# Kernel optimization log

Hardware: AMD Instinct MI355X
Metric: run time of the kernel (lower is better)

## Reference

```python
import jax, jax.numpy as jnp
import numpy as np

H, W = 40, 40
PC_MIN_X, PC_MIN_Y = -51.2, -51.2
DIM_X, DIM_Y = 102.4, 102.4  # pc_range[3:] - pc_range[:3] (x, y)
EFF_MIN, EFF_MAX = 1.0, 6.0


def _grids():
    # np.meshgrid(range(W), range(H)) with 'xy' indexing, then reshape(-1)
    ww = jnp.tile(jnp.arange(W, dtype=jnp.float32), H)
    hh = jnp.repeat(jnp.arange(H, dtype=jnp.float32), W)
    x = (ww + 0.5) / W * DIM_X + PC_MIN_X
    y = (hh + 0.5) / H * DIM_Y + PC_MIN_Y
    return jnp.stack([x, y], axis=1)  # [G=1600, 2]


def _corners(centers, dims, angles):
    # center_to_corner_box2d: unit-square corners scaled, rotated, translated. [M,4,2]
    cn = jnp.array([[-0.5, -0.5], [-0.5, 0.5], [0.5, 0.5], [0.5, -0.5]], dtype=centers.dtype)
    corners = dims[:, None, :] * cn[None]  # [M,4,2]
    c, s = jnp.cos(angles), jnp.sin(angles)
    rot = jnp.stack([jnp.stack([c, -s], -1), jnp.stack([s, c], -1)], -2)  # [M,2,2]
    corners = jnp.einsum('mij,mkj->mki', rot, corners)
    return corners + centers[:, None, :]


def _points_in_poly(points, corners):
    # points [G,2], corners [4,2] -> [G] bool (inside convex quad, sign-consistent cross)
    edges = jnp.roll(corners, -1, axis=0) - corners  # [4,2]
    rel = points[:, None, :] - corners[None]  # [G,4,2]
    cross = edges[None, :, 0] * rel[..., 1] - edges[None, :, 1] * rel[..., 0]  # [G,4]
    return jnp.all(cross >= 0, axis=1) | jnp.all(cross <= 0, axis=1)


def _assign(grids, corners, centers):
    # Sequential per-box grid assignment with the original's overwrite-to-(-1) dedup rule.
    M = corners.shape[0]

    def step(flag, xs):
        i, crn, ctr = xs
        inside = _points_in_poly(grids, crn)
        dist = jnp.sum((grids - ctr) ** 2, axis=1)
        mask = inside.at[jnp.argmin(dist)].set(True)  # always include nearest grid to center
        all_free = jnp.all((~mask) | (flag == -1))
        new_flag = jnp.where(mask, jnp.where(all_free | (flag == -1), i, -1), flag)
        return new_flag, None

    flag0 = -jnp.ones(grids.shape[0], dtype=jnp.int32)
    flag, _ = jax.lax.scan(step, flag0, (jnp.arange(M, dtype=jnp.int32), corners, centers))
    return flag  # [G]


def _forward(atten_map, gt_bboxes):
    B, G, D = atten_map.shape
    M = gt_bboxes.shape[1]
    grids = _grids()
    centers = gt_bboxes[..., :2]
    l, w = gt_bboxes[..., 3], gt_bboxes[..., 4]
    ratio_l = jnp.clip(DIM_X / W / l, EFF_MIN, EFF_MAX)
    ratio_w = jnp.clip(DIM_Y / H / w, EFF_MIN, EFF_MAX)
    eff_dims = jnp.stack([l * ratio_l, w * ratio_w], axis=-1)  # [B,M,2]
    angles = gt_bboxes[..., 6]
    corners = jax.vmap(_corners)(centers, eff_dims, angles)  # [B,M,4,2]
    flags = jax.vmap(lambda c, ct: _assign(grids, c, ct))(corners, centers)  # [B,G]

    # var over feature dim (torch.var default unbiased, ddof=1) per grid cell
    v = jnp.var(atten_map, axis=2, ddof=1)  # [B,G]
    onehot = (flags[:, :, None] == jnp.arange(M, dtype=flags.dtype)[None, None, :])  # [B,G,M]
    counts = onehot.sum(axis=1)  # [B,M]
    sums = jnp.einsum('bg,bgm->bm', v, onehot.astype(v.dtype))
    means = jnp.where(counts > 0, sums / jnp.maximum(counts, 1).astype(v.dtype), 0.0)
    var_loss = -jnp.sum(means)
    pos_num = jnp.maximum(jnp.sum(counts > 0), 1).astype(v.dtype)
    return var_loss / pos_num


def setup_inputs() -> dict:
    key = jax.random.key(0)
    k1, k2 = jax.random.split(key)
    B, G, D, M = 16, 1600, 2048, 64
    atten_map = jax.random.uniform(k1, (B, G, D), dtype=jnp.float32)
    u = jax.random.uniform(k2, (B, M, 7), dtype=jnp.float32)
    xy = u[..., :2] * 80.0 - 40.0          # centers inside pc_range
    z = u[..., 2:3] * 4.0 - 3.0
    lwh = u[..., 3:6] * 7.0 + 1.0          # box sizes in [1, 8] m
    yaw = u[..., 6:7] * (2.0 * np.pi) - np.pi
    gt_bboxes = jnp.concatenate([xy, z, lwh, yaw], axis=-1)
    return {"atten_map": atten_map, "gt_bboxes": gt_bboxes}


def reference(atten_map, gt_bboxes):
    return _forward(atten_map, gt_bboxes)
```

## Files before the change

### kernel.cpp

```cpp
#include <hip/hip_runtime.h>

#define NB 16
#define NG 1600
#define NM 64
#define ND 2048

typedef float floatx4 __attribute__((ext_vector_type(4)));

__global__ __launch_bounds__(256) void var_kernel(const float* __restrict__ atten,
                                                  float* __restrict__ v,
                                                  float* __restrict__ acc) {
    if (blockIdx.x == 0 && threadIdx.x == 0) {
        acc[0] = 0.0f; acc[1] = 0.0f; ((int*)acc)[2] = 0;
    }
    const int wave = threadIdx.x >> 6;
    const int lane = threadIdx.x & 63;
    const int bg = blockIdx.x * 4 + wave;
    const floatx4* p = (const floatx4*)(atten + (size_t)bg * ND);
    double s = 0.0, ss = 0.0;
#pragma unroll
    for (int k = 0; k < 8; ++k) {
        floatx4 f = __builtin_nontemporal_load(p + lane + 64 * k);
        double x0 = f.x, x1 = f.y, x2 = f.z, x3 = f.w;
        s += (x0 + x1) + (x2 + x3);
        ss += (x0 * x0 + x1 * x1) + (x2 * x2 + x3 * x3);
    }
#pragma unroll
    for (int off = 32; off > 0; off >>= 1) {
        s += __shfl_down(s, off, 64);
        ss += __shfl_down(ss, off, 64);
    }
    if (lane == 0)
        v[bg] = (float)((ss - s * s / (double)ND) / (double)(ND - 1));
}

__device__ __forceinline__ int axis_argmin(float c) {
    float u = (c + 51.2f) / 2.56f - 0.5f;
    int i0 = (int)floorf(u) - 1;
    if (i0 < 0) i0 = 0;
    if (i0 > 37) i0 = 37;
    int best_i = i0;
    float best_d = 3.4e38f;
#pragma unroll
    for (int k = 0; k < 3; ++k) {
        int i = i0 + k;
        float p = (i + 0.5f) / 40.0f * 102.4f - 51.2f;
        float d = p - c;
        float d2 = d * d;
        if (d2 < best_d) { best_d = d2; best_i = i; }
    }
    return best_i;
}

__global__ __launch_bounds__(512) void assign_kernel(const float* __restrict__ gt,
                                                     const float* __restrict__ v,
                                                     float* __restrict__ acc,
                                                     float* __restrict__ out) {
    __shared__ float s_kx[NM][4], s_ky[NM][4];
    __shared__ int   s_gmin[NM];
    __shared__ float s_sum[NM];
    __shared__ int   s_cnt[NM];

    const int b = blockIdx.x;
    const int t = threadIdx.x;
    const float* bb = gt + (size_t)b * NM * 7;

    if (t < NM) {
        const float cx = bb[t * 7 + 0], cy = bb[t * 7 + 1];
        const float l = bb[t * 7 + 3], w = bb[t * 7 + 4];
        const float ang = bb[t * 7 + 6];
        float rl = 2.56f / l; rl = fminf(fmaxf(rl, 1.0f), 6.0f);
        float rw = 2.56f / w; rw = fminf(fmaxf(rw, 1.0f), 6.0f);
        const float el = l * rl, ew = w * rw;
        const float c = cosf(ang), s = sinf(ang);
        const float cnx[4] = {-0.5f, -0.5f, 0.5f, 0.5f};
        const float cny[4] = {-0.5f, 0.5f, 0.5f, -0.5f};
#pragma unroll
        for (int k = 0; k < 4; ++k) {
            const float lx = el * cnx[k], ly = ew * cny[k];
            s_kx[t][k] = c * lx - s * ly + cx;
            s_ky[t][k] = s * lx + c * ly + cy;
        }
        s_gmin[t] = axis_argmin(cy) * 40 + axis_argmin(cx);
        s_sum[t] = 0.0f; s_cnt[t] = 0;
    }
    __syncthreads();

    int   flg[4];
    float ppx[4], ppy[4];
#pragma unroll
    for (int k = 0; k < 4; ++k) {
        const int g = t + 512 * k;
        flg[k] = -1;
        if (g < NG) {
            const int wi = g % 40, hi = g / 40;
            ppx[k] = (wi + 0.5f) / 40.0f * 102.4f - 51.2f;
            ppy[k] = (hi + 0.5f) / 40.0f * 102.4f - 51.2f;
        }
    }
    for (int m = 0; m < NM; ++m) {
        const float kx0 = s_kx[m][0], kx1 = s_kx[m][1], kx2 = s_kx[m][2], kx3 = s_kx[m][3];
        const float ky0 = s_ky[m][0], ky1 = s_ky[m][1], ky2 = s_ky[m][2], ky3 = s_ky[m][3];
        const float e0x = kx1 - kx0, e0y = ky1 - ky0;
        const float e1x = kx2 - kx1, e1y = ky2 - ky1;
        const float e2x = kx3 - kx2, e2y = ky3 - ky2;
        const float e3x = kx0 - kx3, e3y = ky0 - ky3;
        const int gm = s_gmin[m];
#pragma unroll
        for (int k = 0; k < 4; ++k) {
            const int g = t + 512 * k;
            if (g < NG) {
                const float px = ppx[k], py = ppy[k];
                const float c0 = e0x * (py - ky0) - e0y * (px - kx0);
                const float c1 = e1x * (py - ky1) - e1y * (px - kx1);
                const float c2 = e2x * (py - ky2) - e2y * (px - kx2);
                const float c3 = e3x * (py - ky3) - e3y * (px - kx3);
                const bool inside =
                    (c0 >= 0.f && c1 >= 0.f && c2 >= 0.f && c3 >= 0.f) ||
                    (c0 <= 0.f && c1 <= 0.f && c2 <= 0.f && c3 <= 0.f);
                if (inside || g == gm) flg[k] = (flg[k] == -1) ? m : -1;
            }
        }
    }

    const float* vb = v + (size_t)b * NG;
#pragma unroll
    for (int k = 0; k < 4; ++k) {
        const int g = t + 512 * k;
        if (g < NG && flg[k] >= 0) {
            atomicAdd(&s_sum[flg[k]], vb[g]);
            atomicAdd(&s_cnt[flg[k]], 1);
        }
    }
    __syncthreads();

    if (t < NM) {
        float mean = (s_cnt[t] > 0) ? (s_sum[t] / (float)s_cnt[t]) : 0.0f;
        float pos  = (s_cnt[t] > 0) ? 1.0f : 0.0f;
#pragma unroll
        for (int off = 32; off > 0; off >>= 1) {
            mean += __shfl_down(mean, off, 64);
            pos  += __shfl_down(pos, off, 64);
        }
        if (t == 0) {
            atomicAdd(&acc[0], mean);
            atomicAdd(&acc[1], pos);
            __threadfence();
            int old = atomicAdd((int*)acc + 2, 1);
            if (old == NB - 1) {
                float S = atomicAdd(&acc[0], 0.0f);
                float P = atomicAdd(&acc[1], 0.0f);
                out[0] = -S / fmaxf(P, 1.0f);
            }
        }
    }
}

extern "C" void kernel_launch(void* const* d_in, const int* in_sizes, int n_in,
                              void* d_out, int out_size, void* d_ws, size_t ws_size,
                              hipStream_t stream) {
    const float* atten = (const float*)d_in[0];
    const float* gt    = (const float*)d_in[1];
    float* out = (float*)d_out;

    float* v   = (float*)d_ws;
    float* acc = v + NB * NG;

    hipLaunchKernelGGL(var_kernel,    dim3(NB * NG / 4), dim3(256), 0, stream, atten, v, acc);
    hipLaunchKernelGGL(assign_kernel, dim3(NB),          dim3(512), 0, stream, gt, v, acc, out);
}
```

Measured before the change: 303.1 us.

## Split assign kernel across grid-cell chunks with global atomic per-box reduction

The assign kernel now launches five blocks per batch, each handling 320 grid cells with one cell per thread, instead of a single 512-thread block looping over four cells per thread. Per-box sums and counts are accumulated into global arrays with atomics. The last block, detected by a ticket counter, computes the means and the final loss. This spreads the sequential 64-box loop over more compute units, at the cost of extra global atomics and a final cross-block reduction.

```diff
diff --git a/kernel.cpp b/kernel.cpp
--- a/kernel.cpp
+++ b/kernel.cpp
@@ -9,9 +9,12 @@
 
 __global__ __launch_bounds__(256) void var_kernel(const float* __restrict__ atten,
                                                   float* __restrict__ v,
-                                                  float* __restrict__ acc) {
-    if (blockIdx.x == 0 && threadIdx.x == 0) {
-        acc[0] = 0.0f; acc[1] = 0.0f; ((int*)acc)[2] = 0;
+                                                  float* __restrict__ gsum,
+                                                  int* __restrict__ gcnt,
+                                                  int* __restrict__ ticket) {
+    if (blockIdx.x == 0) {
+        for (int i = threadIdx.x; i < NB * NM; i += 256) { gsum[i] = 0.0f; gcnt[i] = 0; }
+        if (threadIdx.x == 0) *ticket = 0;
     }
     const int wave = threadIdx.x >> 6;
     const int lane = threadIdx.x & 63;
@@ -52,17 +55,23 @@
     return best_i;
 }
 
-__global__ __launch_bounds__(512) void assign_kernel(const float* __restrict__ gt,
+__global__ __launch_bounds__(320) void assign_kernel(const float* __restrict__ gt,
                                                      const float* __restrict__ v,
-                                                     float* __restrict__ acc,
+                                                     float* __restrict__ gsum,
+                                                     int* __restrict__ gcnt,
+                                                     int* __restrict__ ticket,
                                                      float* __restrict__ out) {
     __shared__ float s_kx[NM][4], s_ky[NM][4];
     __shared__ int   s_gmin[NM];
     __shared__ float s_sum[NM];
     __shared__ int   s_cnt[NM];
+    __shared__ int   s_last;
+    __shared__ float s_redS[5], s_redP[5];
 
     const int b = blockIdx.x;
+    const int q = blockIdx.y;
     const int t = threadIdx.x;
+    const int g = q * 320 + t;
     const float* bb = gt + (size_t)b * NM * 7;
 
     if (t < NM) {
@@ -86,72 +95,59 @@
     }
     __syncthreads();
 
-    int   flg[4];
-    float ppx[4], ppy[4];
-#pragma unroll
-    for (int k = 0; k < 4; ++k) {
-        const int g = t + 512 * k;
-        flg[k] = -1;
-        if (g < NG) {
-            const int wi = g % 40, hi = g / 40;
-            ppx[k] = (wi + 0.5f) / 40.0f * 102.4f - 51.2f;
-            ppy[k] = (hi + 0.5f) / 40.0f * 102.4f - 51.2f;
-        }
-    }
+    const int wi = g % 40, hi = g / 40;
+    const float px = (wi + 0.5f) / 40.0f * 102.4f - 51.2f;
+    const float py = (hi + 0.5f) / 40.0f * 102.4f - 51.2f;
+    int flg = -1;
     for (int m = 0; m < NM; ++m) {
         const float kx0 = s_kx[m][0], kx1 = s_kx[m][1], kx2 = s_kx[m][2], kx3 = s_kx[m][3];
         const float ky0 = s_ky[m][0], ky1 = s_ky[m][1], ky2 = s_ky[m][2], ky3 = s_ky[m][3];
-        const float e0x = kx1 - kx0, e0y = ky1 - ky0;
-        const float e1x = kx2 - kx1, e1y = ky2 - ky1;
-        const float e2x = kx3 - kx2, e2y = ky3 - ky2;
-        const float e3x = kx0 - kx3, e3y = ky0 - ky3;
-        const int gm = s_gmin[m];
-#pragma unroll
-        for (int k = 0; k < 4; ++k) {
-            const int g = t + 512 * k;
-            if (g < NG) {
-                const float px = ppx[k], py = ppy[k];
-                const float c0 = e0x * (py - ky0) - e0y * (px - kx0);
-                const float c1 = e1x * (py - ky1) - e1y * (px - kx1);
-                const float c2 = e2x * (py - ky2) - e2y * (px - kx2);
-                const float c3 = e3x * (py - ky3) - e3y * (px - kx3);
-                const bool inside =
-                    (c0 >= 0.f && c1 >= 0.f && c2 >= 0.f && c3 >= 0.f) ||
-                    (c0 <= 0.f && c1 <= 0.f && c2 <= 0.f && c3 <= 0.f);
-                if (inside || g == gm) flg[k] = (flg[k] == -1) ? m : -1;
-            }
-        }
+        const float c0 = (kx1 - kx0) * (py - ky0) - (ky1 - ky0) * (px - kx0);
+        const float c1 = (kx2 - kx1) * (py - ky1) - (ky2 - ky1) * (px - kx1);
+        const float c2 = (kx3 - kx2) * (py - ky2) - (ky3 - ky2) * (px - kx2);
+        const float c3 = (kx0 - kx3) * (py - ky3) - (ky0 - ky3) * (px - kx3);
+        const bool inside =
+            (c0 >= 0.f && c1 >= 0.f && c2 >= 0.f && c3 >= 0.f) ||
+            (c0 <= 0.f && c1 <= 0.f && c2 <= 0.f && c3 <= 0.f);
+        if (inside || g == s_gmin[m]) flg = (flg == -1) ? m : -1;
     }
 
-    const float* vb = v + (size_t)b * NG;
-#pragma unroll
-    for (int k = 0; k < 4; ++k) {
-        const int g = t + 512 * k;
-        if (g < NG && flg[k] >= 0) {
-            atomicAdd(&s_sum[flg[k]], vb[g]);
-            atomicAdd(&s_cnt[flg[k]], 1);
-        }
+    if (flg >= 0) {
+        atomicAdd(&s_sum[flg], v[(size_t)b * NG + g]);
+        atomicAdd(&s_cnt[flg], 1);
     }
     __syncthreads();
 
-    if (t < NM) {
-        float mean = (s_cnt[t] > 0) ? (s_sum[t] / (float)s_cnt[t]) : 0.0f;
-        float pos  = (s_cnt[t] > 0) ? 1.0f : 0.0f;
+    if (t < NM && s_cnt[t] > 0) {
+        atomicAdd(&gsum[b * NM + t], s_sum[t]);
+        atomicAdd(&gcnt[b * NM + t], s_cnt[t]);
+    }
+    __threadfence();
+    __syncthreads();
+    if (t == 0) s_last = atomicAdd(ticket, 1);
+    __syncthreads();
+
+    if (s_last == NB * 5 - 1) {
+        __threadfence();
+        float S = 0.0f, P = 0.0f;
+        for (int i = t; i < NB * NM; i += 320) {
+            int   c = __hip_atomic_load(&gcnt[i], __ATOMIC_RELAXED, __HIP_MEMORY_SCOPE_AGENT);
+            float s = __hip_atomic_load(&gsum[i], __ATOMIC_RELAXED, __HIP_MEMORY_SCOPE_AGENT);
+            if (c > 0) { S += s / (float)c; P += 1.0f; }
+        }
 #pragma unroll
         for (int off = 32; off > 0; off >>= 1) {
-            mean += __shfl_down(mean, off, 64);
-            pos  += __shfl_down(pos, off, 64);
+            S += __shfl_down(S, off, 64);
+            P += __shfl_down(P, off, 64);
         }
+        const int wv = t >> 6, ln = t & 63;
+        if (ln == 0) { s_redS[wv] = S; s_redP[wv] = P; }
+        __syncthreads();
         if (t == 0) {
-            atomicAdd(&acc[0], mean);
-            atomicAdd(&acc[1], pos);
-            __threadfence();
-            int old = atomicAdd((int*)acc + 2, 1);
-            if (old == NB - 1) {
-                float S = atomicAdd(&acc[0], 0.0f);
-                float P = atomicAdd(&acc[1], 0.0f);
-                out[0] = -S / fmaxf(P, 1.0f);
-            }
+            float ST = 0.0f, PT = 0.0f;
+#pragma unroll
+            for (int w = 0; w < 5; ++w) { ST += s_redS[w]; PT += s_redP[w]; }
+            out[0] = -ST / fmaxf(PT, 1.0f);
         }
     }
 }
@@ -163,9 +159,13 @@
     const float* gt    = (const float*)d_in[1];
     float* out = (float*)d_out;
 
-    float* v   = (float*)d_ws;
-    float* acc = v + NB * NG;
+    float* v      = (float*)d_ws;
+    float* gsum   = v + NB * NG;
+    int*   gcnt   = (int*)(gsum + NB * NM);
+    int*   ticket = gcnt + NB * NM;
 
-    hipLaunchKernelGGL(var_kernel,    dim3(NB * NG / 4), dim3(256), 0, stream, atten, v, acc);
-    hipLaunchKernelGGL(assign_kernel, dim3(NB),          dim3(512), 0, stream, gt, v, acc, out);
+    hipLaunchKernelGGL(var_kernel,    dim3(NB * NG / 4), dim3(256), 0, stream,
+                       atten, v, gsum, gcnt, ticket);
+    hipLaunchKernelGGL(assign_kernel, dim3(NB, 5),       dim3(320), 0, stream,
+                       gt, v, gsum, gcnt, ticket, out);
 }
```

After: 288.1 us. 1.05x faster.
